# Kernel optimization log

Hardware: AMD Instinct MI355X
Metric: run time of the kernel (lower is better)

Reference implementation:

```python
import jax, jax.numpy as jnp
import numpy as np

D = 1024
H = 16
HD = D // H
FF = 4096
EPS = 1e-5
B, L = 8, 1024

def setup_inputs() -> dict:
    key = jax.random.key(0)
    ks = jax.random.split(key, 12)
    s = lambda k, shape: jax.random.normal(k, shape, dtype=jnp.float32) * (shape[0] ** -0.5)
    return {
        "x": jax.random.normal(ks[0], (B, L, D), dtype=jnp.float32),
        "attention_mask": jnp.ones((B, L), dtype=jnp.int32),
        "wq": s(ks[1], (D, D)), "bq": jnp.zeros((D,), jnp.float32),
        "wk": s(ks[2], (D, D)), "bk": jnp.zeros((D,), jnp.float32),
        "wv": s(ks[3], (D, D)), "bv": jnp.zeros((D,), jnp.float32),
        "wo": s(ks[4], (D, D)), "bo": jnp.zeros((D,), jnp.float32),
        "ln1_s": jnp.ones((D,), jnp.float32), "ln1_b": jnp.zeros((D,), jnp.float32),
        "ln2_s": jnp.ones((D,), jnp.float32), "ln2_b": jnp.zeros((D,), jnp.float32),
        "w1": s(ks[5], (D, FF)), "b1": jnp.zeros((FF,), jnp.float32),
        "w2": s(ks[6], (FF, D)), "b2": jnp.zeros((D,), jnp.float32),
    }

def _layer_norm(x, scale, bias):
    mu = jnp.mean(x, axis=-1, keepdims=True)
    var = jnp.mean(jnp.square(x - mu), axis=-1, keepdims=True)
    return (x - mu) * jax.lax.rsqrt(var + EPS) * scale + bias

def _quick_gelu(x):
    return x * jax.nn.sigmoid(1.702 * x)

def reference(x, attention_mask, wq, bq, wk, bk, wv, bv, wo, bo,
              ln1_s, ln1_b, ln2_s, ln2_b, w1, b1, w2, b2):
    Bc, Lc, Dc = x.shape
    scale = HD ** -0.5
    # --- attention block (pre-LN) ---
    h = _layer_norm(x, ln1_s, ln1_b)
    to_heads = lambda t: t.reshape(Bc, Lc, H, HD).transpose(0, 2, 1, 3)
    q = to_heads(h @ wq + bq)
    k = to_heads(h @ wk + bk)
    v = to_heads(h @ wv + bv)
    scores = jnp.einsum('bhqd,bhkd->bhqk', q.astype(jnp.float32), k.astype(jnp.float32)) * scale
    fmask = jnp.where(attention_mask[:, None, None, :] > 0, 0.0,
                      jnp.finfo(scores.dtype).min)
    weights = jax.nn.softmax(scores + fmask, axis=-1)
    attn = jnp.einsum('bhqk,bhkd->bhqd', weights, v.astype(jnp.float32))
    attn = attn.transpose(0, 2, 1, 3).reshape(Bc, Lc, Dc).astype(x.dtype)
    x = x + (attn @ wo + bo)
    # --- MLP block (pre-LN) ---
    h = _layer_norm(x, ln2_s, ln2_b)
    h = _quick_gelu(h @ w1 + b1) @ w2 + b2
    return x + h
```

## Files before the change

### kernel.cpp

```cpp
#include <hip/hip_runtime.h>
#include <math.h>

#define D_MODEL 1024
#define N_TOK   8192
#define SEQ_L   1024
#define N_HEAD  16
#define HEAD_D  64
#define FF_DIM  4096

typedef __attribute__((ext_vector_type(8))) short bf16x8;
typedef __attribute__((ext_vector_type(4))) short short4v;
typedef __attribute__((ext_vector_type(2))) int  int2v;
typedef __attribute__((ext_vector_type(4))) float f32x4;

#define MFMA16(a, b, c) __builtin_amdgcn_mfma_f32_16x16x32_bf16((a), (b), (c), 0, 0, 0)

#define GLD16(gp, lp) __builtin_amdgcn_global_load_lds(                      \
    (const __attribute__((address_space(1))) void*)(gp),                     \
    (__attribute__((address_space(3))) void*)(lp), 16, 0, 0)

#if defined(__has_builtin)
#if __has_builtin(__builtin_amdgcn_exp2f)
#define EXP2F(x) __builtin_amdgcn_exp2f(x)
#else
#define EXP2F(x) exp2f(x)
#endif
#else
#define EXP2F(x) exp2f(x)
#endif

__device__ __forceinline__ short f2bf(float f) {
    unsigned u = __float_as_uint(f);
    u += 0x7fffu + ((u >> 16) & 1u);
    return (short)(u >> 16);
}

__device__ __forceinline__ int pack2bf(float a, float b) {
    unsigned ua = __float_as_uint(a) + 0x8000u;
    unsigned ub = __float_as_uint(b) + 0x8000u;
    return __builtin_amdgcn_perm(ub, ua, 0x07060302u);
}

__global__ __launch_bounds__(256) void ln_kernel(const float* __restrict__ x,
                                                 const float* __restrict__ g,
                                                 const float* __restrict__ b,
                                                 short* __restrict__ o)
{
    int t = blockIdx.x;
    const float* xr = x + (size_t)t * D_MODEL;
    short* orow = o + (size_t)t * D_MODEL;
    float vals[4];
    float lsum = 0.f, lsq = 0.f;
#pragma unroll
    for (int i = 0; i < 4; i++) {
        float v = xr[threadIdx.x + i * 256];
        vals[i] = v; lsum += v; lsq += v * v;
    }
#pragma unroll
    for (int off = 32; off > 0; off >>= 1) {
        lsum += __shfl_down(lsum, off);
        lsq  += __shfl_down(lsq,  off);
    }
    __shared__ float red[8];
    int wid = threadIdx.x >> 6, lane = threadIdx.x & 63;
    if (lane == 0) { red[wid] = lsum; red[4 + wid] = lsq; }
    __syncthreads();
    if (threadIdx.x == 0) {
        red[0] = red[0] + red[1] + red[2] + red[3];
        red[4] = red[4] + red[5] + red[6] + red[7];
    }
    __syncthreads();
    float mean = red[0] * (1.f / D_MODEL);
    float var  = red[4] * (1.f / D_MODEL) - mean * mean;
    float inv  = rsqrtf(var + 1e-5f);
#pragma unroll
    for (int i = 0; i < 4; i++) {
        int c = threadIdx.x + i * 256;
        orow[c] = f2bf((vals[i] - mean) * inv * g[c] + b[c]);
    }
}

__global__ __launch_bounds__(256) void prep_kernel(
    const float* __restrict__ wq, const float* __restrict__ wk,
    const float* __restrict__ wv, const float* __restrict__ wo,
    const float* __restrict__ w1, const float* __restrict__ w2,
    const int*   __restrict__ amask,
    short* __restrict__ wqkvt, short* __restrict__ wot,
    short* __restrict__ w1t,  short* __restrict__ w2t,
    float* __restrict__ fmask)
{
    int id = blockIdx.x;
    if (id >= 12288) {
        int i = (id - 12288) * 256 + threadIdx.x;
        fmask[i] = (amask[i] > 0) ? 0.f : -1e30f;
        return;
    }
    const float* src; short* dst; int R, C, tloc, csh;
    if (id < 4096) {
        int wsel = id >> 10; tloc = id & 1023; R = 1024; C = 1024; csh = 5;
        src = (wsel == 0) ? wq : (wsel == 1) ? wk : (wsel == 2) ? wv : wo;
        dst = (wsel == 3) ? wot : (wqkvt + (size_t)wsel * 1024 * 1024);
    } else if (id < 8192) {
        tloc = id - 4096; R = 1024; C = 4096; csh = 7; src = w1; dst = w1t;
    } else {
        tloc = id - 8192; R = 4096; C = 1024; csh = 5; src = w2; dst = w2t;
    }
    int ty = tloc >> csh, tx = tloc & ((1 << csh) - 1);
    int r0 = ty * 32, c0 = tx * 32;
    __shared__ float t[32][33];
    int tid = threadIdx.x;
#pragma unroll
    for (int i = 0; i < 4; i++) {
        int idx = i * 256 + tid;
        int r = idx >> 5, c = idx & 31;
        t[r][c] = src[(size_t)(r0 + r) * C + c0 + c];
    }
    __syncthreads();
#pragma unroll
    for (int i = 0; i < 4; i++) {
        int idx = i * 256 + tid;
        int rr = idx >> 5, cc = idx & 31;
        dst[(size_t)(c0 + rr) * R + r0 + cc] = f2bf(t[cc][rr]);
    }
}

__global__ __launch_bounds__(256) void gemm_bf16(
    const short* __restrict__ A, int lda,
    const short* __restrict__ Bt, int ldb,
    const float* __restrict__ bias,
    const float* __restrict__ bias2,
    const float* __restrict__ bias3,
    const float* __restrict__ resid,
    float* __restrict__ Cf, short* __restrict__ Cb, short* __restrict__ Cvt,
    int ldc, int K, int act, int qkv, int gx)
{
    __shared__ __align__(16) short sA[128 * 64];
    __shared__ __align__(16) short sB[128 * 64];
    const int tid = threadIdx.x;
    const int lane = tid & 63, wave = tid >> 6;
    const int quad = lane >> 4, l15 = lane & 15;

    const int id = blockIdx.x;
    const int xcd = id & 7, j = id >> 3;
    const int bx = j % gx, by = xcd + 8 * (j / gx);
    const int bm = by * 128, bn = bx * 128;
    const int wm = (wave >> 1) * 64, wn = (wave & 1) * 64;

    const int lr = lane >> 3;
    const int lc = (lane & 7) ^ lr;
    const int sw = l15 & 7;

    f32x4 acc[4][4];
#pragma unroll
    for (int i = 0; i < 4; i++)
#pragma unroll
        for (int jj = 0; jj < 4; jj++) acc[i][jj] = (f32x4){0.f, 0.f, 0.f, 0.f};

    for (int k0 = 0; k0 < K; k0 += 64) {
        __syncthreads();
#pragma unroll
        for (int c = 0; c < 4; c++) {
            int cid = wave * 4 + c;
            GLD16(A  + (size_t)(bm + cid * 8 + lr) * lda + k0 + lc * 8,
                  &sA[cid * 512]);
            GLD16(Bt + (size_t)(bn + cid * 8 + lr) * ldb + k0 + lc * 8,
                  &sB[cid * 512]);
        }
        __syncthreads();
#pragma unroll
        for (int ko = 0; ko < 2; ko++) {
            bf16x8 af[4], bfr[4];
#pragma unroll
            for (int mt = 0; mt < 4; mt++) {
                int row = wm + mt * 16 + l15;
                af[mt] = *(const bf16x8*)&sA[(row * 8 + ((ko * 4 + quad) ^ sw)) * 8];
            }
#pragma unroll
            for (int nt = 0; nt < 4; nt++) {
                int row = wn + nt * 16 + l15;
                bfr[nt] = *(const bf16x8*)&sB[(row * 8 + ((ko * 4 + quad) ^ sw)) * 8];
            }
#pragma unroll
            for (int mt = 0; mt < 4; mt++)
#pragma unroll
                for (int nt = 0; nt < 4; nt++)
                    acc[mt][nt] = MFMA16(af[mt], bfr[nt], acc[mt][nt]);
        }
    }

#pragma unroll
    for (int mt = 0; mt < 4; mt++)
#pragma unroll
        for (int nt = 0; nt < 4; nt++) {
            int row0 = bm + wm + mt * 16 + quad * 4;
            int col  = bn + wn + nt * 16 + l15;
            if (qkv) {
                int seg = col >> 10, cloc = col & 1023;
                const float* bp = (seg == 0) ? bias : (seg == 1) ? bias2 : bias3;
                float bval = bp[cloc];
                if (seg == 2) {
                    int bb = row0 >> 10, l0 = row0 & 1023;
                    size_t page = (size_t)(bb * N_HEAD + (cloc >> 6)) * HEAD_D + (cloc & 63);
                    short4v pk = { f2bf(acc[mt][nt][0] + bval), f2bf(acc[mt][nt][1] + bval),
                                   f2bf(acc[mt][nt][2] + bval), f2bf(acc[mt][nt][3] + bval) };
                    *(short4v*)&Cvt[page * SEQ_L + l0] = pk;
                } else {
                    short* dst = Cb + (size_t)seg * ((size_t)N_TOK * D_MODEL);
#pragma unroll
                    for (int r = 0; r < 4; r++)
                        dst[(size_t)(row0 + r) * D_MODEL + cloc] = f2bf(acc[mt][nt][r] + bval);
                }
            } else {
#pragma unroll
                for (int r = 0; r < 4; r++) {
                    int row = row0 + r;
                    float v = acc[mt][nt][r] + bias[col];
                    if (act) v = v / (1.f + __expf(-1.702f * v));
                    if (resid) v += resid[(size_t)row * ldc + col];
                    if (Cb) Cb[(size_t)row * ldc + col] = f2bf(v);
                    else    Cf[(size_t)row * ldc + col] = v;
                }
            }
        }
}

__global__ __launch_bounds__(256) void attn_kernel(
    const short* __restrict__ Q, const short* __restrict__ Kb,
    const short* __restrict__ Vt, const float* __restrict__ fmask,
    short* __restrict__ O)
{
    __shared__ __align__(16) short sK[8192];
    __shared__ __align__(16) short sV[8192];
    __shared__ __align__(16) short sP[4][16 * 136];
    __shared__ __align__(16) float sAl[4][20];

    const int g = blockIdx.x;
    const int xcd = g & 7, slot = g >> 3;
    const int qt = slot & 15, bhl = slot >> 4;
    const int bh = xcd * 16 + bhl;
    const int b = bh >> 4, h = bh & 15;

    const int tid = threadIdx.x;
    const int wave = tid >> 6, lane = tid & 63;
    const int quad = lane >> 4, l15 = lane & 15;

    const int qbase = b * SEQ_L + qt * 64;
    const short* qp = Q + (size_t)(qbase + wave * 16 + l15) * D_MODEL + h * HEAD_D + quad * 8;
    bf16x8 qf0 = *(const bf16x8*)qp;
    bf16x8 qf1 = *(const bf16x8*)(qp + 32);

    const short* Kbh = Kb + (size_t)b * SEQ_L * D_MODEL + h * HEAD_D;
    const short* Vbh = Vt + (size_t)(b * N_HEAD + h) * HEAD_D * SEQ_L;
    const float* mk  = fmask + b * SEQ_L;

    f32x4 o4[4];
#pragma unroll
    for (int nt = 0; nt < 4; nt++) o4[nt] = (f32x4){0.f, 0.f, 0.f, 0.f};
    float mrow = -1e30f, lrow = 0.f;
    short* pslab = &sP[wave][0];
    const float CSC = 0.125f * 1.4426950408889634f;

    for (int kt = 0; kt < SEQ_L / 128; kt++) {
        __syncthreads();
#pragma unroll
        for (int j = 0; j < 4; j++) {
            int cid = wave * 4 + j;
            int kc = cid >> 1, key0 = (cid & 1) << 6;
            GLD16(Kbh + (size_t)(kt * 128 + key0 + lane) * D_MODEL + kc * 8,
                  &sK[cid * 512]);
            GLD16(Vbh + (size_t)lane * SEQ_L + kt * 128 + cid * 8,
                  &sV[cid * 512]);
        }
        __syncthreads();

        f32x4 mkv[8];
#pragma unroll
        for (int sub = 0; sub < 8; sub++)
            mkv[sub] = *(const f32x4*)&mk[kt * 128 + sub * 16 + quad * 4];

        f32x4 s[8];
#pragma unroll
        for (int sub = 0; sub < 8; sub++) {
            bf16x8 kf0 = *(const bf16x8*)&sK[(quad * 128 + sub * 16 + l15) * 8];
            bf16x8 kf1 = *(const bf16x8*)&sK[((quad + 4) * 128 + sub * 16 + l15) * 8];
            s[sub] = (f32x4){0.f, 0.f, 0.f, 0.f};
            s[sub] = MFMA16(kf0, qf0, s[sub]);
            s[sub] = MFMA16(kf1, qf1, s[sub]);
        }
#pragma unroll
        for (int sub = 0; sub < 8; sub++)
#pragma unroll
            for (int r = 0; r < 4; r++) s[sub][r] = s[sub][r] * CSC + mkv[sub][r];

        f32x4 mx4 = s[0];
#pragma unroll
        for (int sub = 1; sub < 8; sub++)
#pragma unroll
            for (int r = 0; r < 4; r++) mx4[r] = fmaxf(mx4[r], s[sub][r]);
        float pmax = fmaxf(fmaxf(mx4[0], mx4[1]), fmaxf(mx4[2], mx4[3]));
        pmax = fmaxf(pmax, __shfl_xor(pmax, 16));
        pmax = fmaxf(pmax, __shfl_xor(pmax, 32));
        float mnew = fmaxf(mrow, pmax);
        float alpha = EXP2F(mrow - mnew);
        mrow = mnew;
        if (quad == 0) sAl[wave][l15] = alpha;

        float ls = 0.f;
#pragma unroll
        for (int sub = 0; sub < 8; sub++) {
            float p0 = EXP2F(s[sub][0] - mnew);
            float p1 = EXP2F(s[sub][1] - mnew);
            float p2 = EXP2F(s[sub][2] - mnew);
            float p3 = EXP2F(s[sub][3] - mnew);
            ls += (p0 + p1) + (p2 + p3);
            int2v pk = { pack2bf(p0, p1), pack2bf(p2, p3) };
            *(int2v*)&pslab[l15 * 136 + sub * 16 + quad * 4] = pk;
        }
        ls += __shfl_xor(ls, 16);
        ls += __shfl_xor(ls, 32);
        lrow = lrow * alpha + ls;

        f32x4 av = *(const f32x4*)&sAl[wave][quad * 4];
#pragma unroll
        for (int nt = 0; nt < 4; nt++)
#pragma unroll
            for (int r = 0; r < 4; r++) o4[nt][r] *= av[r];

        bf16x8 pf[4];
#pragma unroll
        for (int c = 0; c < 4; c++)
            pf[c] = *(const bf16x8*)&pslab[l15 * 136 + c * 32 + quad * 8];
#pragma unroll
        for (int nt = 0; nt < 4; nt++)
#pragma unroll
            for (int c = 0; c < 4; c++) {
                bf16x8 vfr = *(const bf16x8*)&sV[((c * 4 + quad) * 64 + nt * 16 + l15) * 8];
                o4[nt] = MFMA16(pf[c], vfr, o4[nt]);
            }
    }
    if (quad == 0) sAl[wave][l15] = 1.f / lrow;
    __syncthreads();
    f32x4 iv = *(const f32x4*)&sAl[wave][quad * 4];
#pragma unroll
    for (int nt = 0; nt < 4; nt++)
#pragma unroll
        for (int r = 0; r < 4; r++)
            O[(size_t)(qbase + wave * 16 + quad * 4 + r) * D_MODEL
              + h * HEAD_D + nt * 16 + l15] = f2bf(o4[nt][r] * iv[r]);
}

extern "C" void kernel_launch(void* const* d_in, const int* in_sizes, int n_in,
                              void* d_out, int out_size, void* d_ws, size_t ws_size,
                              hipStream_t stream)
{
    const float* x     = (const float*)d_in[0];
    const int*   amask = (const int*)  d_in[1];
    const float* wq    = (const float*)d_in[2];
    const float* bq    = (const float*)d_in[3];
    const float* wk    = (const float*)d_in[4];
    const float* bk    = (const float*)d_in[5];
    const float* wv    = (const float*)d_in[6];
    const float* bv    = (const float*)d_in[7];
    const float* wo    = (const float*)d_in[8];
    const float* bo    = (const float*)d_in[9];
    const float* ln1s  = (const float*)d_in[10];
    const float* ln1b  = (const float*)d_in[11];
    const float* ln2s  = (const float*)d_in[12];
    const float* ln2b  = (const float*)d_in[13];
    const float* w1    = (const float*)d_in[14];
    const float* b1    = (const float*)d_in[15];
    const float* w2    = (const float*)d_in[16];
    const float* b2    = (const float*)d_in[17];
    float* out = (float*)d_out;

    char* w = (char*)d_ws;
    short* wqkvt = (short*)(w + (size_t)0);
    short* wot   = (short*)(w + ((size_t)6  << 20));
    short* w1t   = (short*)(w + ((size_t)8  << 20));
    short* w2t   = (short*)(w + ((size_t)16 << 20));
    short* hb    = (short*)(w + ((size_t)24 << 20));
    short* qb    = (short*)(w + ((size_t)40 << 20));
    short* kbf   = (short*)(w + ((size_t)56 << 20));
    short* attnb = (short*)(w + ((size_t)72 << 20));
    short* vtb   = (short*)(w + ((size_t)88 << 20));
    short* ffb   = qb;
    float* fmaskb = (float*)d_out;

    dim3 blk(256);

    prep_kernel<<<dim3(12320), blk, 0, stream>>>(wq, wk, wv, wo, w1, w2, amask,
                                                 wqkvt, wot, w1t, w2t, fmaskb);

    ln_kernel<<<N_TOK, blk, 0, stream>>>(x, ln1s, ln1b, hb);

    gemm_bf16<<<dim3(24 * 64), blk, 0, stream>>>(
        hb, 1024, wqkvt, 1024, bq, bk, bv, nullptr,
        nullptr, qb, vtb, 1024, 1024, 0, 1, 24);

    attn_kernel<<<dim3(2048), blk, 0, stream>>>(qb, kbf, vtb, fmaskb, attnb);

    gemm_bf16<<<dim3(8 * 64), blk, 0, stream>>>(
        attnb, 1024, wot, 1024, bo, nullptr, nullptr, x,
        out, nullptr, nullptr, 1024, 1024, 0, 0, 8);

    ln_kernel<<<N_TOK, blk, 0, stream>>>(out, ln2s, ln2b, hb);

    gemm_bf16<<<dim3(32 * 64), blk, 0, stream>>>(
        hb, 1024, w1t, 1024, b1, nullptr, nullptr, nullptr,
        nullptr, ffb, nullptr, 4096, 1024, 1, 0, 32);
    gemm_bf16<<<dim3(8 * 64), blk, 0, stream>>>(
        ffb, 4096, w2t, 4096, b2, nullptr, nullptr, out,
        out, nullptr, nullptr, 1024, 4096, 0, 0, 8);
}
```

Measured before the change: 588.8 us.

## Double-buffer LDS tiles in bf16 GEMM to overlap global loads with MFMA

Splits the GEMM's shared-memory A/B tiles into two buffers. The next K-slice is prefetched with global_load_lds while MFMAs run on the current slice, which also drops one barrier per iteration. Base row pointers are hoisted out of the loop. This doubles LDS use per block, which may lower occupancy, and the compiler may still insert waits that serialize the prefetch.

New measurement: 574.4 us. 2.5% less time.

```diff
diff --git a/kernel.cpp b/kernel.cpp
--- a/kernel.cpp
+++ b/kernel.cpp
@@ -134,8 +134,8 @@
     float* __restrict__ Cf, short* __restrict__ Cb, short* __restrict__ Cvt,
     int ldc, int K, int act, int qkv, int gx)
 {
-    __shared__ __align__(16) short sA[128 * 64];
-    __shared__ __align__(16) short sB[128 * 64];
+    __shared__ __align__(16) short sA[2][128 * 64];
+    __shared__ __align__(16) short sB[2][128 * 64];
     const int tid = threadIdx.x;
     const int lane = tid & 63, wave = tid >> 6;
     const int quad = lane >> 4, l15 = lane & 15;
@@ -150,35 +150,48 @@
     const int lc = (lane & 7) ^ lr;
     const int sw = l15 & 7;
 
+    const short* Ab = A  + (size_t)(bm + wave * 32 + lr) * lda + lc * 8;
+    const short* Bb = Bt + (size_t)(bn + wave * 32 + lr) * ldb + lc * 8;
+
     f32x4 acc[4][4];
 #pragma unroll
     for (int i = 0; i < 4; i++)
 #pragma unroll
         for (int jj = 0; jj < 4; jj++) acc[i][jj] = (f32x4){0.f, 0.f, 0.f, 0.f};
 
-    for (int k0 = 0; k0 < K; k0 += 64) {
+    const int nk = K >> 6;
+#pragma unroll
+    for (int c = 0; c < 4; c++) {
+        int cid = wave * 4 + c;
+        GLD16(Ab + (size_t)(c * 8) * lda, &sA[0][cid * 512]);
+        GLD16(Bb + (size_t)(c * 8) * ldb, &sB[0][cid * 512]);
+    }
+
+    for (int ki = 0; ki < nk; ki++) {
         __syncthreads();
-#pragma unroll
-        for (int c = 0; c < 4; c++) {
-            int cid = wave * 4 + c;
-            GLD16(A  + (size_t)(bm + cid * 8 + lr) * lda + k0 + lc * 8,
-                  &sA[cid * 512]);
-            GLD16(Bt + (size_t)(bn + cid * 8 + lr) * ldb + k0 + lc * 8,
-                  &sB[cid * 512]);
-        }
-        __syncthreads();
+        if (ki + 1 < nk) {
+            int k0 = (ki + 1) << 6, nb = (ki + 1) & 1;
+#pragma unroll
+            for (int c = 0; c < 4; c++) {
+                int cid = wave * 4 + c;
+                GLD16(Ab + (size_t)(c * 8) * lda + k0, &sA[nb][cid * 512]);
+                GLD16(Bb + (size_t)(c * 8) * ldb + k0, &sB[nb][cid * 512]);
+            }
+        }
+        const short* cA = sA[ki & 1];
+        const short* cB = sB[ki & 1];
 #pragma unroll
         for (int ko = 0; ko < 2; ko++) {
             bf16x8 af[4], bfr[4];
 #pragma unroll
             for (int mt = 0; mt < 4; mt++) {
                 int row = wm + mt * 16 + l15;
-                af[mt] = *(const bf16x8*)&sA[(row * 8 + ((ko * 4 + quad) ^ sw)) * 8];
+                af[mt] = *(const bf16x8*)&cA[(row * 8 + ((ko * 4 + quad) ^ sw)) * 8];
             }
 #pragma unroll
             for (int nt = 0; nt < 4; nt++) {
                 int row = wn + nt * 16 + l15;
-                bfr[nt] = *(const bf16x8*)&sB[(row * 8 + ((ko * 4 + quad) ^ sw)) * 8];
+                bfr[nt] = *(const bf16x8*)&cB[(row * 8 + ((ko * 4 + quad) ^ sw)) * 8];
             }
 #pragma unroll
             for (int mt = 0; mt < 4; mt++)
```
